# Optimization experiments

Measured on AMD Instinct MI355X. Metric: run time of the kernel, lower is better.

Reference implementation:

```python
import jax, jax.numpy as jnp
import numpy as np

IN_F = 1024
OUT_F = 1024
GRID = 8
TOKENS = 8192


def setup_inputs() -> dict:
    key = jax.random.key(0)
    k_x, k_w, k_b, k_s = jax.random.split(key, 4)
    x = jax.random.normal(k_x, (TOKENS, IN_F), dtype=jnp.float32)
    # kaiming_uniform_(nonlinearity='linear'): bound = sqrt(3/fan_in)
    bound_w = float(np.sqrt(3.0 / IN_F))
    W = jax.random.uniform(k_w, (OUT_F, IN_F), minval=-bound_w, maxval=bound_w, dtype=jnp.float32)
    # nn.Linear default bias init: U(-1/sqrt(fan_in), 1/sqrt(fan_in))
    bound_b = float(1.0 / np.sqrt(IN_F))
    b = jax.random.uniform(k_b, (OUT_F,), minval=-bound_b, maxval=bound_b, dtype=jnp.float32)
    spline_weight = jax.random.uniform(k_s, (OUT_F, IN_F, GRID), minval=-0.1, maxval=0.1, dtype=jnp.float32)
    grid = jnp.linspace(-3.0, 3.0, GRID, dtype=jnp.float32)
    return {"x": x, "W": W, "b": b, "spline_weight": spline_weight, "grid": grid}


def reference(x, W, b, spline_weight, grid):
    grid_size = spline_weight.shape[-1]
    # base path: Linear(silu(x))
    base = jnp.einsum('ti,oi->to', jax.nn.silu(x), W) + b
    # RBF basis: [tokens, in_features, grid_size]
    denom = 2.0 / (grid_size - 1) + 1e-05
    basis = jnp.exp(-(((x[..., None] - grid) / denom) ** 2))
    spline = jnp.einsum('tig,oig->to', basis, spline_weight)
    return base + spline
```

## Files before the change

### kernel.cpp

```cpp
#include <hip/hip_runtime.h>
#include <hip/hip_bf16.h>

#define IN_F   1024
#define OUT_F  1024
#define TOKENS 8192
#define KTOT   9216
#define KHALF  4608
#define NTILE  72

typedef __attribute__((ext_vector_type(8))) short  bf16x8;
typedef __attribute__((ext_vector_type(4))) float  f32x4;

template<int M> struct ModeT { static constexpr int value = M; };

__device__ __forceinline__ unsigned int f2bf(float f) {
    union { float f; unsigned int u; } v; v.f = f;
    unsigned int r = v.u + 0x7fffu + ((v.u >> 16) & 1u);
    return r >> 16;
}

__global__ __launch_bounds__(256)
void prep_a_kernel(const float* __restrict__ x, const float* __restrict__ grid,
                   unsigned short* __restrict__ A)
{
    int idx = blockIdx.x * blockDim.x + threadIdx.x;
    int t = idx >> 10;
    int i = idx & 1023;
    float xv = x[idx];
    float sil = xv / (1.0f + __expf(-xv));
    A[(size_t)t * KTOT + i] = (unsigned short)f2bf(sil);

    const float invd = 1.0f / (2.0f / 7.0f + 1e-5f);
    unsigned int h[8];
    #pragma unroll
    for (int g = 0; g < 8; ++g) {
        float d = (xv - grid[g]) * invd;
        h[g] = f2bf(__expf(-d * d));
    }
    uint4 pk;
    pk.x = h[0] | (h[1] << 16);
    pk.y = h[2] | (h[3] << 16);
    pk.z = h[4] | (h[5] << 16);
    pk.w = h[6] | (h[7] << 16);
    *reinterpret_cast<uint4*>(&A[(size_t)t * KTOT + IN_F + (size_t)i * 8]) = pk;
}

__global__ __launch_bounds__(256)
void prep_b_kernel(const float* __restrict__ W, const float* __restrict__ spl,
                   unsigned short* __restrict__ B)
{
    int idx = blockIdx.x * blockDim.x + threadIdx.x;
    int o  = idx / (KTOT / 8);
    int c8 = idx - o * (KTOT / 8);
    const float* src = (c8 < IN_F / 8)
        ? (W   + (size_t)o * IN_F     + (size_t)c8 * 8)
        : (spl + (size_t)o * IN_F * 8 + (size_t)(c8 - IN_F / 8) * 8);
    const float4* s4 = reinterpret_cast<const float4*>(src);
    float4 lo = s4[0], hi = s4[1];
    uint4 pk;
    pk.x = f2bf(lo.x) | (f2bf(lo.y) << 16);
    pk.y = f2bf(lo.z) | (f2bf(lo.w) << 16);
    pk.z = f2bf(hi.x) | (f2bf(hi.y) << 16);
    pk.w = f2bf(hi.z) | (f2bf(hi.w) << 16);
    *reinterpret_cast<uint4*>(&B[(size_t)o * KTOT + (size_t)c8 * 8]) = pk;
}

#define GLOAD(src, dst) __builtin_amdgcn_global_load_lds( \
    (const __attribute__((address_space(1))) void*)(src),  \
    (__attribute__((address_space(3))) void*)(dst), 16, 0, 0)
#define SBAR()  __builtin_amdgcn_s_barrier()
#define SCH0()  __builtin_amdgcn_sched_barrier(0)
#define VMC0()  asm volatile("s_waitcnt vmcnt(0)" ::: "memory")

__global__ __launch_bounds__(512, 2)
void gemm_kan2(const unsigned short* __restrict__ A,
               const unsigned short* __restrict__ B,
               float* __restrict__ P, int rows)
{
    __shared__ char lds[131072];

    const int bid  = blockIdx.x;
    const int sk   = bid & 1;
    const int bn   = (bid >> 1) & 3;
    const int bm   = bid >> 3;
    const int tid  = threadIdx.x;
    const int wave = tid >> 6, lane = tid & 63;
    const int wr   = wave >> 2, wc = wave & 3;
    const int fr   = lane & 15, kg = lane >> 4;
    const int sw   = fr & 7;
    const int koff[2] = { (kg ^ sw) * 16, ((4 | kg) ^ sw) * 16 };
    const int k0 = sk * KHALF;

    const int trow = tid >> 3;
    const int ksrc = ((tid & 7) ^ (trow & 7)) * 8;
    const unsigned short* gA = A + (size_t)(bm * 256 + trow) * KTOT + k0 + ksrc;
    const unsigned short* gB = B + (size_t)(bn * 256 + trow) * KTOT + k0 + ksrc;
    const size_t R64 = (size_t)64 * KTOT;

    f32x4 acc[8][4];
    const f32x4 zero = {0.f, 0.f, 0.f, 0.f};
    #pragma unroll
    for (int m = 0; m < 8; ++m)
        #pragma unroll
        for (int n = 0; n < 4; ++n) acc[m][n] = zero;

    {
        char* dA = lds + tid * 16;
        char* dB = lds + 65536 + tid * 16;
        GLOAD(gA,           dA);           GLOAD(gA + R64,     dA + 8192);
        GLOAD(gA + 2 * R64, dA + 16384);   GLOAD(gA + 3 * R64, dA + 24576);
        GLOAD(gB,           dB);           GLOAD(gB + R64,     dB + 8192);
        GLOAD(gB + 2 * R64, dB + 16384);   GLOAD(gB + 3 * R64, dB + 24576);
        gA += 64; gB += 64;
    }
    VMC0(); SBAR(); SCH0();

    const int aOff = (wr * 64 + fr) * 128;
    const int bOff = (wc * 32 + fr) * 128;

    bf16x8 af[4][2], bfLo[2][2], bfHi[2][2];
    int u = 0;

    auto tile = [&](auto mC) {
        constexpr int MODE = decltype(mC)::value;
        char* bufA = lds + (u & 1) * 32768;
        char* bufB = lds + 65536 + (u & 1) * 32768;

        #pragma unroll
        for (int mi = 0; mi < 4; ++mi)
            #pragma unroll
            for (int ks = 0; ks < 2; ++ks)
                af[mi][ks] = *(const bf16x8*)(bufA + aOff + mi * 2048 + koff[ks]);
        #pragma unroll
        for (int ni = 0; ni < 2; ++ni)
            #pragma unroll
            for (int ks = 0; ks < 2; ++ks) {
                bfLo[ni][ks] = *(const bf16x8*)(bufB + bOff + ni * 2048 + koff[ks]);
                bfHi[ni][ks] = *(const bf16x8*)(bufB + bOff + 16384 + ni * 2048 + koff[ks]);
            }

        if constexpr (MODE == 0) {
            char* dA = lds + ((u & 1) ^ 1) * 32768 + tid * 16;
            char* dB = lds + 65536 + ((u & 1) ^ 1) * 32768 + tid * 16;
            GLOAD(gA,           dA);           GLOAD(gA + R64,     dA + 8192);
            GLOAD(gA + 2 * R64, dA + 16384);   GLOAD(gA + 3 * R64, dA + 24576);
            GLOAD(gB,           dB);           GLOAD(gB + R64,     dB + 8192);
            GLOAD(gB + 2 * R64, dB + 16384);   GLOAD(gB + 3 * R64, dB + 24576);
            gA += 64; gB += 64;
        }
        SCH0();

        __builtin_amdgcn_s_setprio(1);
        #pragma unroll
        for (int mi = 0; mi < 4; ++mi)
            #pragma unroll
            for (int ni = 0; ni < 2; ++ni)
                #pragma unroll
                for (int ks = 0; ks < 2; ++ks)
                    acc[mi][ni] = __builtin_amdgcn_mfma_f32_16x16x32_bf16(
                        af[mi][ks], bfLo[ni][ks], acc[mi][ni], 0, 0, 0);
        __builtin_amdgcn_s_setprio(0);

        __builtin_amdgcn_s_setprio(1);
        #pragma unroll
        for (int mi = 0; mi < 4; ++mi)
            #pragma unroll
            for (int ni = 0; ni < 2; ++ni)
                #pragma unroll
                for (int ks = 0; ks < 2; ++ks)
                    acc[mi][2 + ni] = __builtin_amdgcn_mfma_f32_16x16x32_bf16(
                        af[mi][ks], bfHi[ni][ks], acc[mi][2 + ni], 0, 0, 0);
        __builtin_amdgcn_s_setprio(0);

        #pragma unroll
        for (int mi = 0; mi < 4; ++mi)
            #pragma unroll
            for (int ks = 0; ks < 2; ++ks)
                af[mi][ks] = *(const bf16x8*)(bufA + aOff + 16384 + mi * 2048 + koff[ks]);

        __builtin_amdgcn_s_setprio(1);
        #pragma unroll
        for (int mi = 0; mi < 4; ++mi)
            #pragma unroll
            for (int ni = 0; ni < 2; ++ni)
                #pragma unroll
                for (int ks = 0; ks < 2; ++ks)
                    acc[4 + mi][ni] = __builtin_amdgcn_mfma_f32_16x16x32_bf16(
                        af[mi][ks], bfLo[ni][ks], acc[4 + mi][ni], 0, 0, 0);
        __builtin_amdgcn_s_setprio(0);

        __builtin_amdgcn_s_setprio(1);
        #pragma unroll
        for (int mi = 0; mi < 4; ++mi)
            #pragma unroll
            for (int ni = 0; ni < 2; ++ni)
                #pragma unroll
                for (int ks = 0; ks < 2; ++ks)
                    acc[4 + mi][2 + ni] = __builtin_amdgcn_mfma_f32_16x16x32_bf16(
                        af[mi][ks], bfHi[ni][ks], acc[4 + mi][2 + ni], 0, 0, 0);
        __builtin_amdgcn_s_setprio(0);

        SCH0();
        if constexpr (MODE == 0) {
            VMC0();
            SBAR(); SCH0();
        }
    };

    for (u = 0; u < NTILE - 1; ++u) tile(ModeT<0>{});
    tile(ModeT<1>{});

    float* Pp = P + (size_t)sk * rows * OUT_F;
    const size_t orow0 = (size_t)bm * 256 + (size_t)wr * 64;
    const int    ocol0 = bn * 256 + wc * 32;
    #pragma unroll
    for (int n = 0; n < 4; ++n) {
        const int col = ocol0 + (n & 1) * 16 + (n >> 1) * 128 + fr;
        #pragma unroll
        for (int m = 0; m < 8; ++m) {
            const size_t r0 = orow0 + (m & 3) * 16 + (m >> 2) * 128 + kg * 4;
            #pragma unroll
            for (int j = 0; j < 4; ++j)
                Pp[(r0 + j) * OUT_F + col] = acc[m][n][j];
        }
    }
}

__global__ __launch_bounds__(256)
void reduce_kan(const float* __restrict__ P, const float* __restrict__ bias,
                float* __restrict__ out, int n4, int skStride4)
{
    const float4* p0 = (const float4*)P;
    const float4* p1 = p0 + skStride4;
    const float4* bv = (const float4*)bias;
    float4* o = (float4*)out;
    for (int i = blockIdx.x * blockDim.x + threadIdx.x; i < n4;
         i += gridDim.x * blockDim.x) {
        float4 a = p0[i], b = p1[i], c = bv[i & 255];
        float4 r;
        r.x = a.x + b.x + c.x;  r.y = a.y + b.y + c.y;
        r.z = a.z + b.z + c.z;  r.w = a.w + b.w + c.w;
        o[i] = r;
    }
}

extern "C" void kernel_launch(void* const* d_in, const int* in_sizes, int n_in,
                              void* d_out, int out_size, void* d_ws, size_t ws_size,
                              hipStream_t stream)
{
    const float* x    = (const float*)d_in[0];
    const float* W    = (const float*)d_in[1];
    const float* bias = (const float*)d_in[2];
    const float* spl  = (const float*)d_in[3];
    const float* grid = (const float*)d_in[4];
    float* out = (float*)d_out;

    unsigned short* Bw = (unsigned short*)d_ws;
    unsigned short* Aw = Bw + (size_t)OUT_F * KTOT;

    const size_t bBytes = (size_t)OUT_F * KTOT * 2;
    size_t avail = ws_size > bBytes ? ws_size - bBytes : 0;
    long maxRows = (long)(avail / 26624);
    int chunk = (maxRows >= TOKENS) ? TOKENS : (int)((maxRows / 256) * 256);
    if (chunk < 256) chunk = 256;
    float* Pp = (float*)(Aw + (size_t)chunk * KTOT);

    prep_b_kernel<<<(OUT_F * (KTOT / 8)) / 256, 256, 0, stream>>>(W, spl, Bw);

    for (int t0 = 0; t0 < TOKENS; t0 += chunk) {
        int rows = (TOKENS - t0 < chunk) ? (TOKENS - t0) : chunk;
        prep_a_kernel<<<(rows * IN_F) / 256, 256, 0, stream>>>(
            x + (size_t)t0 * IN_F, grid, Aw);
        gemm_kan2<<<(rows >> 8) * 8, 512, 0, stream>>>(Aw, Bw, Pp, rows);
        int n4 = rows * 256;
        int rblocks = (n4 + 255) / 256; if (rblocks > 2048) rblocks = 2048;
        reduce_kan<<<rblocks, 256, 0, stream>>>(
            Pp, bias, out + (size_t)t0 * OUT_F, n4, n4);
    }
}
```

Measured before the change: 195.2 us.

## Fuse prep kernels and interleave LDS reads with MFMAs via sched_group_barrier

The A and B prep kernels become one launch whenever the full token range fits in the workspace, which removes one kernel launch and lets the two memory-bound conversions share the GPU. Inside the GEMM tile loop, the bfHi and second-half A fragment LDS reads move between MFMA groups. The global-to-LDS prefetch now comes after the reads, and sched_group_barrier hints interleave DS reads, VMEM loads and MFMAs. The aim is to hide LDS and global-load latency behind matrix instructions, at the cost of depending on compiler scheduling and possibly higher register pressure.

```diff
diff --git a/kernel.cpp b/kernel.cpp
--- a/kernel.cpp
+++ b/kernel.cpp
@@ -19,11 +19,10 @@
     return r >> 16;
 }
 
-__global__ __launch_bounds__(256)
-void prep_a_kernel(const float* __restrict__ x, const float* __restrict__ grid,
-                   unsigned short* __restrict__ A)
-{
-    int idx = blockIdx.x * blockDim.x + threadIdx.x;
+__device__ __forceinline__ void prep_a_body(int idx, const float* __restrict__ x,
+                                            const float* __restrict__ grid,
+                                            unsigned short* __restrict__ A)
+{
     int t = idx >> 10;
     int i = idx & 1023;
     float xv = x[idx];
@@ -45,11 +44,10 @@
     *reinterpret_cast<uint4*>(&A[(size_t)t * KTOT + IN_F + (size_t)i * 8]) = pk;
 }
 
-__global__ __launch_bounds__(256)
-void prep_b_kernel(const float* __restrict__ W, const float* __restrict__ spl,
-                   unsigned short* __restrict__ B)
-{
-    int idx = blockIdx.x * blockDim.x + threadIdx.x;
+__device__ __forceinline__ void prep_b_body(int idx, const float* __restrict__ W,
+                                            const float* __restrict__ spl,
+                                            unsigned short* __restrict__ B)
+{
     int o  = idx / (KTOT / 8);
     int c8 = idx - o * (KTOT / 8);
     const float* src = (c8 < IN_F / 8)
@@ -65,12 +63,39 @@
     *reinterpret_cast<uint4*>(&B[(size_t)o * KTOT + (size_t)c8 * 8]) = pk;
 }
 
+__global__ __launch_bounds__(256)
+void prep_fused(const float* __restrict__ x, const float* __restrict__ grid,
+                const float* __restrict__ W, const float* __restrict__ spl,
+                unsigned short* __restrict__ A, unsigned short* __restrict__ B)
+{
+    int b = blockIdx.x;
+    if (b < (TOKENS * IN_F) / 256)
+        prep_a_body(b * 256 + threadIdx.x, x, grid, A);
+    else
+        prep_b_body((b - (TOKENS * IN_F) / 256) * 256 + threadIdx.x, W, spl, B);
+}
+
+__global__ __launch_bounds__(256)
+void prep_a_kernel(const float* __restrict__ x, const float* __restrict__ grid,
+                   unsigned short* __restrict__ A)
+{
+    prep_a_body(blockIdx.x * blockDim.x + threadIdx.x, x, grid, A);
+}
+
+__global__ __launch_bounds__(256)
+void prep_b_kernel(const float* __restrict__ W, const float* __restrict__ spl,
+                   unsigned short* __restrict__ B)
+{
+    prep_b_body(blockIdx.x * blockDim.x + threadIdx.x, W, spl, B);
+}
+
 #define GLOAD(src, dst) __builtin_amdgcn_global_load_lds( \
     (const __attribute__((address_space(1))) void*)(src),  \
     (__attribute__((address_space(3))) void*)(dst), 16, 0, 0)
 #define SBAR()  __builtin_amdgcn_s_barrier()
 #define SCH0()  __builtin_amdgcn_sched_barrier(0)
 #define VMC0()  asm volatile("s_waitcnt vmcnt(0)" ::: "memory")
+#define SGB(m, n) __builtin_amdgcn_sched_group_barrier((m), (n), 0)
 
 __global__ __launch_bounds__(512, 2)
 void gemm_kan2(const unsigned short* __restrict__ A,
@@ -134,10 +159,40 @@
         #pragma unroll
         for (int ni = 0; ni < 2; ++ni)
             #pragma unroll
-            for (int ks = 0; ks < 2; ++ks) {
+            for (int ks = 0; ks < 2; ++ks)
                 bfLo[ni][ks] = *(const bf16x8*)(bufB + bOff + ni * 2048 + koff[ks]);
+
+        __builtin_amdgcn_s_setprio(1);
+
+        #pragma unroll
+        for (int mi = 0; mi < 4; ++mi)
+            #pragma unroll
+            for (int ni = 0; ni < 2; ++ni)
+                #pragma unroll
+                for (int ks = 0; ks < 2; ++ks)
+                    acc[mi][ni] = __builtin_amdgcn_mfma_f32_16x16x32_bf16(
+                        af[mi][ks], bfLo[ni][ks], acc[mi][ni], 0, 0, 0);
+
+        #pragma unroll
+        for (int ni = 0; ni < 2; ++ni)
+            #pragma unroll
+            for (int ks = 0; ks < 2; ++ks)
                 bfHi[ni][ks] = *(const bf16x8*)(bufB + bOff + 16384 + ni * 2048 + koff[ks]);
-            }
+
+        #pragma unroll
+        for (int mi = 0; mi < 4; ++mi)
+            #pragma unroll
+            for (int ni = 0; ni < 2; ++ni)
+                #pragma unroll
+                for (int ks = 0; ks < 2; ++ks)
+                    acc[mi][2 + ni] = __builtin_amdgcn_mfma_f32_16x16x32_bf16(
+                        af[mi][ks], bfHi[ni][ks], acc[mi][2 + ni], 0, 0, 0);
+
+        #pragma unroll
+        for (int mi = 0; mi < 4; ++mi)
+            #pragma unroll
+            for (int ks = 0; ks < 2; ++ks)
+                af[mi][ks] = *(const bf16x8*)(bufA + aOff + 16384 + mi * 2048 + koff[ks]);
 
         if constexpr (MODE == 0) {
             char* dA = lds + ((u & 1) ^ 1) * 32768 + tid * 16;
@@ -148,37 +203,7 @@
             GLOAD(gB + 2 * R64, dB + 16384);   GLOAD(gB + 3 * R64, dB + 24576);
             gA += 64; gB += 64;
         }
-        SCH0();
-
-        __builtin_amdgcn_s_setprio(1);
-        #pragma unroll
-        for (int mi = 0; mi < 4; ++mi)
-            #pragma unroll
-            for (int ni = 0; ni < 2; ++ni)
-                #pragma unroll
-                for (int ks = 0; ks < 2; ++ks)
-                    acc[mi][ni] = __builtin_amdgcn_mfma_f32_16x16x32_bf16(
-                        af[mi][ks], bfLo[ni][ks], acc[mi][ni], 0, 0, 0);
-        __builtin_amdgcn_s_setprio(0);
-
-        __builtin_amdgcn_s_setprio(1);
-        #pragma unroll
-        for (int mi = 0; mi < 4; ++mi)
-            #pragma unroll
-            for (int ni = 0; ni < 2; ++ni)
-                #pragma unroll
-                for (int ks = 0; ks < 2; ++ks)
-                    acc[mi][2 + ni] = __builtin_amdgcn_mfma_f32_16x16x32_bf16(
-                        af[mi][ks], bfHi[ni][ks], acc[mi][2 + ni], 0, 0, 0);
-        __builtin_amdgcn_s_setprio(0);
-
-        #pragma unroll
-        for (int mi = 0; mi < 4; ++mi)
-            #pragma unroll
-            for (int ks = 0; ks < 2; ++ks)
-                af[mi][ks] = *(const bf16x8*)(bufA + aOff + 16384 + mi * 2048 + koff[ks]);
-
-        __builtin_amdgcn_s_setprio(1);
+
         #pragma unroll
         for (int mi = 0; mi < 4; ++mi)
             #pragma unroll
@@ -187,9 +212,7 @@
                 for (int ks = 0; ks < 2; ++ks)
                     acc[4 + mi][ni] = __builtin_amdgcn_mfma_f32_16x16x32_bf16(
                         af[mi][ks], bfLo[ni][ks], acc[4 + mi][ni], 0, 0, 0);
-        __builtin_amdgcn_s_setprio(0);
-
-        __builtin_amdgcn_s_setprio(1);
+
         #pragma unroll
         for (int mi = 0; mi < 4; ++mi)
             #pragma unroll
@@ -198,9 +221,20 @@
                 for (int ks = 0; ks < 2; ++ks)
                     acc[4 + mi][2 + ni] = __builtin_amdgcn_mfma_f32_16x16x32_bf16(
                         af[mi][ks], bfHi[ni][ks], acc[4 + mi][2 + ni], 0, 0, 0);
+
         __builtin_amdgcn_s_setprio(0);
 
-        SCH0();
+        SGB(0x100, 12);
+        #pragma unroll
+        for (int i = 0; i < 12; ++i) { SGB(0x8, 2); SGB(0x100, 1); }
+        if constexpr (MODE == 0) {
+            #pragma unroll
+            for (int i = 0; i < 8; ++i) { SGB(0x8, 2); SGB(0x30, 1); }
+        } else {
+            SGB(0x8, 16);
+        }
+        SGB(0x8, 24);
+
         if constexpr (MODE == 0) {
             VMC0();
             SBAR(); SCH0();
@@ -265,16 +299,23 @@
     if (chunk < 256) chunk = 256;
     float* Pp = (float*)(Aw + (size_t)chunk * KTOT);
 
-    prep_b_kernel<<<(OUT_F * (KTOT / 8)) / 256, 256, 0, stream>>>(W, spl, Bw);
-
-    for (int t0 = 0; t0 < TOKENS; t0 += chunk) {
-        int rows = (TOKENS - t0 < chunk) ? (TOKENS - t0) : chunk;
-        prep_a_kernel<<<(rows * IN_F) / 256, 256, 0, stream>>>(
-            x + (size_t)t0 * IN_F, grid, Aw);
-        gemm_kan2<<<(rows >> 8) * 8, 512, 0, stream>>>(Aw, Bw, Pp, rows);
-        int n4 = rows * 256;
-        int rblocks = (n4 + 255) / 256; if (rblocks > 2048) rblocks = 2048;
-        reduce_kan<<<rblocks, 256, 0, stream>>>(
-            Pp, bias, out + (size_t)t0 * OUT_F, n4, n4);
-    }
-}
+    if (chunk == TOKENS) {
+        prep_fused<<<(TOKENS * IN_F) / 256 + (OUT_F * (KTOT / 8)) / 256,
+                     256, 0, stream>>>(x, grid, W, spl, Aw, Bw);
+        gemm_kan2<<<(TOKENS >> 8) * 8, 512, 0, stream>>>(Aw, Bw, Pp, TOKENS);
+        int n4 = TOKENS * 256;
+        reduce_kan<<<2048, 256, 0, stream>>>(Pp, bias, out, n4, n4);
+    } else {
+        prep_b_kernel<<<(OUT_F * (KTOT / 8)) / 256, 256, 0, stream>>>(W, spl, Bw);
+        for (int t0 = 0; t0 < TOKENS; t0 += chunk) {
+            int rows = (TOKENS - t0 < chunk) ? (TOKENS - t0) : chunk;
+            prep_a_kernel<<<(rows * IN_F) / 256, 256, 0, stream>>>(
+                x + (size_t)t0 * IN_F, grid, Aw);
+            gemm_kan2<<<(rows >> 8) * 8, 512, 0, stream>>>(Aw, Bw, Pp, rows);
+            int n4 = rows * 256;
+            int rblocks = (n4 + 255) / 256; if (rblocks > 2048) rblocks = 2048;
+            reduce_kan<<<rblocks, 256, 0, stream>>>(
+                Pp, bias, out + (size_t)t0 * OUT_F, n4, n4);
+        }
+    }
+}
```

New measurement: 200.8 us. 1.03x slower.
